# Kernel tuning notes

Hardware: AMD Instinct MI355X
Metric: run time of the kernel (lower is better)

Reference implementation:

```python
import jax, jax.numpy as jnp
import numpy as np

B, T, D, H, DK, DV = 2, 2048, 1024, 16, 64, 64
MODEL_SIZE = 1024
NEG_INF = -2.3819763e38
EPS = 1e-6
MAX_WAVELENGTH = 10000


def rms_norm(x, scale):
    # flax nn.RMSNorm over last axis, eps=1e-6, learned scale init to ones
    var = jnp.mean(jnp.square(x), axis=-1, keepdims=True)
    return x * jax.lax.rsqrt(var + EPS) * scale


def apply_rope(x):
    # x: [B, T, H, head_dim]
    *_, seq_len, num_heads, head_dim = x.shape
    fraction = 2 * jnp.arange(0, head_dim // 2) / head_dim
    timescale = MAX_WAVELENGTH ** fraction
    positions = jnp.arange(seq_len, dtype=x.dtype)
    sinusoid_inp = positions[:, None] / timescale[None, :]  # [T, head_dim//2]
    sinusoid_inp = sinusoid_inp[:, None, :]                 # [T, 1, head_dim//2]
    sin = jnp.sin(sinusoid_inp)
    cos = jnp.cos(sinusoid_inp)
    first_half, second_half = jnp.split(x, 2, axis=-1)
    first_part = first_half * cos - second_half * sin
    second_part = second_half * cos + first_half * sin
    return jnp.concatenate([first_part, second_part], axis=-1).astype(x.dtype)


def setup_inputs() -> dict:
    key = jax.random.key(0)
    ks = jax.random.split(key, 12)
    s = 0.02
    return {
        "query": jax.random.normal(ks[0], (B, T, D), jnp.float32),
        "key": jax.random.normal(ks[1], (B, T, D), jnp.float32),
        "value": jax.random.normal(ks[2], (B, T, D), jnp.float32),
        "mask": jnp.ones((B, H, T, T), dtype=bool),
        "Wq": jax.random.normal(ks[3], (D, H * DK), jnp.float32) * s,
        "bq": jnp.zeros((H * DK,), jnp.float32),
        "Wk": jax.random.normal(ks[4], (D, H * DK), jnp.float32) * s,
        "bk": jnp.zeros((H * DK,), jnp.float32),
        "Wv": jax.random.normal(ks[5], (D, H * DV), jnp.float32) * s,
        "bv": jnp.zeros((H * DV,), jnp.float32),
        "Wo": jax.random.normal(ks[6], (H * DV, MODEL_SIZE), jnp.float32) * s,
        "bo": jnp.zeros((MODEL_SIZE,), jnp.float32),
        "gq": jnp.ones((DK,), jnp.float32),
        "gk": jnp.ones((DK,), jnp.float32),
    }


def reference(query, key, value, mask, Wq, bq, Wk, bk, Wv, bv, Wo, bo, gq, gk):
    # Q/K projections with per-head RMSNorm then RoPE
    qh = (query @ Wq + bq).reshape(B, T, H, DK)
    qh = apply_rope(rms_norm(qh, gq))
    kh = (key @ Wk + bk).reshape(B, T, H, DK)
    kh = apply_rope(rms_norm(kh, gk))
    vh = (value @ Wv + bv).reshape(B, T, H, DV)

    logits = jnp.einsum("bthd,bThd->bhtT", qh, kh) / np.sqrt(DK).astype(query.dtype)
    logits = jnp.where(mask, logits, NEG_INF)
    weights = jax.nn.softmax(logits, axis=-1)
    weights = jnp.where(mask, weights, 0)
    attn = jnp.einsum("bhtT,bThd->bthd", weights, vh).reshape(B, T, H * DV)
    return attn @ Wo + bo
```

## Files before the change

kernel.cpp:

```cpp
#include <hip/hip_runtime.h>
#include <hip/hip_bf16.h>
#include <cstdint>
#include <cstddef>


typedef unsigned short ushort_t;
typedef unsigned int uint32;
typedef __bf16 bf16x8 __attribute__((ext_vector_type(8)));
typedef float f32x4 __attribute__((ext_vector_type(4)));

#define DEV static __device__ __forceinline__

DEV ushort_t f2bf(float f){
  uint32 x = __builtin_bit_cast(uint32, f);
  uint32 r = (x + 0x7fffu + ((x >> 16) & 1u)) >> 16;
  return (ushort_t)r;
}
DEV bf16x8 cvt8(f32x4 lo, f32x4 hi){
  bf16x8 r;
#pragma unroll
  for(int j=0;j<4;j++){ r[j] = (__bf16)lo[j]; r[j+4] = (__bf16)hi[j]; }
  return r;
}
DEV void gl_lds16(const ushort_t* g, ushort_t* l){
  __builtin_amdgcn_global_load_lds(
      (const __attribute__((address_space(1))) uint32*)g,
      (__attribute__((address_space(3))) uint32*)l, 16, 0, 0);
}

__global__ __launch_bounds__(256) void cvtbf(const float* __restrict__ x0,
                                             const float* __restrict__ x1,
                                             const float* __restrict__ x2,
                                             ushort_t* __restrict__ y0,
                                             ushort_t* __restrict__ y1,
                                             ushort_t* __restrict__ y2){
  int z = blockIdx.y;
  const float* x = (z==0)?x0:(z==1)?x1:x2;
  ushort_t* y    = (z==0)?y0:(z==1)?y1:y2;
  size_t i = ((size_t)blockIdx.x*256 + threadIdx.x)*8;
  f32x4 lo = *(const f32x4*)(x+i);
  f32x4 hi = *(const f32x4*)(x+i+4);
  *(bf16x8*)(y+i) = cvt8(lo, hi);
}

__global__ __launch_bounds__(256) void wtrans(const float* __restrict__ w0,
                                              const float* __restrict__ w1,
                                              const float* __restrict__ w2,
                                              const float* __restrict__ w3,
                                              ushort_t* __restrict__ wt){
  __shared__ float tile[64][65];
  int z = blockIdx.z;
  const float* W = (z==0)?w0:(z==1)?w1:(z==2)?w2:w3;
  ushort_t* O = wt + (size_t)z * (1024u*1024u);
  int kb = blockIdx.y * 64, nb = blockIdx.x * 64;
  int tr = threadIdx.x >> 4, tc = threadIdx.x & 15;
#pragma unroll
  for(int p=0;p<4;p++){
    int r = tr + p*16;
    f32x4 u = *(const f32x4*)(W + (size_t)(kb + r)*1024 + nb + tc*4);
    tile[r][tc*4+0]=u[0]; tile[r][tc*4+1]=u[1]; tile[r][tc*4+2]=u[2]; tile[r][tc*4+3]=u[3];
  }
  __syncthreads();
#pragma unroll
  for(int p=0;p<4;p++){
    int r = tr + p*16;
    ushort4 u;
    u.x = f2bf(tile[tc*4+0][r]); u.y = f2bf(tile[tc*4+1][r]);
    u.z = f2bf(tile[tc*4+2][r]); u.w = f2bf(tile[tc*4+3][r]);
    *(ushort4*)(O + (size_t)(nb + r)*1024 + kb + tc*4) = u;
  }
}

__global__ __launch_bounds__(256) void gemm128(
    const ushort_t* __restrict__ A0, const ushort_t* __restrict__ A1, const ushort_t* __restrict__ A2,
    const ushort_t* __restrict__ WT,
    const float* __restrict__ b0, const float* __restrict__ b1, const float* __restrict__ b2,
    ushort_t* __restrict__ O0, ushort_t* __restrict__ O1, ushort_t* __restrict__ O2,
    float* __restrict__ OF, int vtz, int f32z)
{
  __shared__ ushort_t As[128*32];
  __shared__ ushort_t Bs[128*32];
  const int K = 1024, N = 1024;
  int z = blockIdx.z;
  const ushort_t* A   = (z==0) ? A0 : (z==1) ? A1 : A2;
  const ushort_t* Bt  = WT + (size_t)z * (1024u*1024u);
  const float* bias   = (z==0) ? b0 : (z==1) ? b1 : b2;
  ushort_t* Cp        = (z==0) ? O0 : (z==1) ? O1 : O2;
  int rowBase = blockIdx.y * 128, colBase = blockIdx.x * 128;
  int tid = threadIdx.x, wave = tid >> 6, lane = tid & 63;
  int lr = lane & 15, lq = lane >> 4;
  int m0 = (wave & 1) * 64, n0 = (wave >> 1) * 64;
  int srow = wave*16 + (lane >> 2);
  int skc  = (lane & 3) * 8;
  const ushort_t* gA = A  + (size_t)(rowBase + srow)*K + skc;
  const ushort_t* gB = Bt + (size_t)(colBase + srow)*K + skc;
  ushort_t* lA = &As[srow*32 + skc];
  ushort_t* lB = &Bs[srow*32 + skc];
  f32x4 acc[4][4] = {};
  for(int kb = 0; kb < K; kb += 32){
    gl_lds16(gA + kb,          lA);
    gl_lds16(gA + kb + 64*K,   lA + 64*32);
    gl_lds16(gB + kb,          lB);
    gl_lds16(gB + kb + 64*K,   lB + 64*32);
    __syncthreads();
    bf16x8 af[4], bfr[4];
#pragma unroll
    for(int mi=0;mi<4;mi++) af[mi]  = *(const bf16x8*)&As[(m0 + mi*16 + lr)*32 + lq*8];
#pragma unroll
    for(int ni=0;ni<4;ni++) bfr[ni] = *(const bf16x8*)&Bs[(n0 + ni*16 + lr)*32 + lq*8];
#pragma unroll
    for(int mi=0;mi<4;mi++)
#pragma unroll
      for(int ni=0;ni<4;ni++)
        acc[mi][ni] = __builtin_amdgcn_mfma_f32_16x16x32_bf16(af[mi], bfr[ni], acc[mi][ni], 0,0,0);
    __syncthreads();
  }
  bool vt = (z == vtz);
  bool f32o = (z == f32z);
#pragma unroll
  for(int ni=0;ni<4;ni++){
    int col = colBase + n0 + ni*16 + lr;
    float bv = bias[col];
#pragma unroll
    for(int mi=0;mi<4;mi++){
      int row = rowBase + m0 + mi*16 + lq*4;
#pragma unroll
      for(int r=0;r<4;r++){
        float v = acc[mi][ni][r] + bv;
        if(f32o){
          OF[(size_t)(row + r)*N + col] = v;
        } else if(!vt){
          Cp[(size_t)(row + r)*N + col] = f2bf(v);
        } else {
          int rw = row + r;
          int bb = rw >> 11, t = rw & 2047, hh = col >> 6, dv = col & 63;
          Cp[((size_t)((bb*16 + hh)*64 + dv))*2048 + t] = f2bf(v);
        }
      }
    }
  }
}

__global__ __launch_bounds__(256) void rmsrope(ushort_t* __restrict__ QH, ushort_t* __restrict__ KH,
                                               const float* __restrict__ gq, const float* __restrict__ gk){
  int wave = threadIdx.x >> 6, lane = threadIdx.x & 63;
  int idx = blockIdx.x * 4 + wave;
  int s = idx >> 16;
  int rem = idx & 65535;
  ushort_t* P = s ? KH : QH;
  const float* G = s ? gk : gq;
  size_t base = (size_t)rem * 64;
  union { uint32 i; float f; } cv0; cv0.i = ((uint32)P[base + lane]) << 16;
  float x = cv0.f;
  float ss = x * x;
#pragma unroll
  for(int d=1; d<64; d<<=1) ss += __shfl_xor(ss, d, 64);
  float rn = rsqrtf(ss * (1.0f/64.0f) + 1e-6f);
  float xn = x * rn * G[lane];
  int i = lane & 31;
  int tpos = (rem >> 4) & 2047;
  float invts = exp2f((float)i * (-13.287712379549449f/32.0f));
  float ang = (float)tpos * invts;
  float sv, cvv;
  sincosf(ang, &sv, &cvv);
  float pr = __shfl_xor(xn, 32, 64);
  float out = (lane < 32) ? (xn*cvv - pr*sv) : (xn*cvv + pr*sv);
  P[base + lane] = f2bf(out);
}

__global__ __launch_bounds__(256, 2) void attn_k(const ushort_t* __restrict__ QH,
                                                 const ushort_t* __restrict__ KH,
                                                 const ushort_t* __restrict__ VT,
                                                 ushort_t* __restrict__ AT){
  __shared__ float sO[4][64][33];
  __shared__ float sM[4][32];
  __shared__ float sL[4][32];
  const float C = 0.18033688011112042f;
  int blk = blockIdx.x;
  int r5 = blk & 31;
  int bh = (r5 & 7)*4 + (r5 >> 3);
  int qt = blk >> 5;
  int b = bh >> 4, h = bh & 15;
  int q0 = qt * 64;
  int tid = threadIdx.x, wave = tid >> 6, lane = tid & 63;
  int lr = lane & 15, lq = lane >> 4;
  size_t tok0 = (size_t)b * 2048;

  bf16x8 qf[2][4];
#pragma unroll
  for(int ks=0;ks<2;ks++)
#pragma unroll
    for(int nt=0;nt<4;nt++){
      size_t e = ((tok0 + q0 + nt*16 + lr)*16 + h)*64 + (size_t)ks*32 + lq*8;
      qf[ks][nt] = *(const bf16x8*)(QH + e);
    }
  f32x4 o[4][4] = {};
  float m[4] = {-1e30f, -1e30f, -1e30f, -1e30f};
  float l[4] = {0.f, 0.f, 0.f, 0.f};
  size_t vbase = ((size_t)(b*16 + h) * 64) * 2048;

  for(int it=0; it<16; ++it){
    int kb = wave*512 + it*32;
    bf16x8 kA[2][2];
#pragma unroll
    for(int mt=0;mt<2;mt++)
#pragma unroll
      for(int ks=0;ks<2;ks++){
        size_t e = ((tok0 + kb + mt*16 + lr)*16 + h)*64 + (size_t)ks*32 + lq*8;
        kA[mt][ks] = *(const bf16x8*)(KH + e);
      }
    bf16x8 vA[4];
#pragma unroll
    for(int dvt=0;dvt<4;dvt++){
      size_t e = vbase + (size_t)(dvt*16 + lr)*2048 + kb + lq*8;
      vA[dvt] = *(const bf16x8*)(VT + e);
    }
    f32x4 s[2][4] = {};
#pragma unroll
    for(int ks=0;ks<2;ks++)
#pragma unroll
      for(int mt=0;mt<2;mt++)
#pragma unroll
        for(int nt=0;nt<4;nt++)
          s[mt][nt] = __builtin_amdgcn_mfma_f32_16x16x32_bf16(kA[mt][ks], qf[ks][nt], s[mt][nt], 0,0,0);

#pragma unroll
    for(int nt=0;nt<4;nt++){
      float mx = s[0][nt][0];
#pragma unroll
      for(int r=1;r<4;r++) mx = fmaxf(mx, s[0][nt][r]);
#pragma unroll
      for(int r=0;r<4;r++) mx = fmaxf(mx, s[1][nt][r]);
      mx = fmaxf(mx, __shfl_xor(mx, 16, 64));
      mx = fmaxf(mx, __shfl_xor(mx, 32, 64));
      float mn = fmaxf(m[nt], mx);
      float al = exp2f((m[nt] - mn) * C);
      m[nt] = mn;
      float rs = 0.f;
#pragma unroll
      for(int mt=0;mt<2;mt++)
#pragma unroll
        for(int r=0;r<4;r++){
          float p = exp2f((s[mt][nt][r] - mn) * C);
          s[mt][nt][r] = p;
          rs += p;
        }
      rs += __shfl_xor(rs, 16, 64);
      rs += __shfl_xor(rs, 32, 64);
      l[nt] = l[nt]*al + rs;
#pragma unroll
      for(int dvt=0;dvt<4;dvt++) o[dvt][nt] *= al;
    }
#pragma unroll
    for(int nt=0;nt<4;nt++){
      bf16x8 pB;
      int srcbase = lr + (lq & 1)*32;
#pragma unroll
      for(int j=0;j<8;j++){
        int src = srcbase + (j>>2)*16;
        float va = __shfl(s[0][nt][j&3], src, 64);
        float vb = __shfl(s[1][nt][j&3], src, 64);
        float pv = (lq >= 2) ? vb : va;
        pB[j] = (__bf16)pv;
      }
#pragma unroll
      for(int dvt=0;dvt<4;dvt++)
        o[dvt][nt] = __builtin_amdgcn_mfma_f32_16x16x32_bf16(vA[dvt], pB, o[dvt][nt], 0,0,0);
    }
  }
#pragma unroll
  for(int p=0;p<2;p++){
    __syncthreads();
#pragma unroll
    for(int ntl=0;ntl<2;ntl++){
      int nt = p*2 + ntl;
      if(lane < 16){ sM[wave][ntl*16+lane] = m[nt]; sL[wave][ntl*16+lane] = l[nt]; }
#pragma unroll
      for(int dvt=0;dvt<4;dvt++)
#pragma unroll
        for(int r=0;r<4;r++)
          sO[wave][dvt*16 + lq*4 + r][ntl*16 + lr] = o[dvt][nt][r];
    }
    __syncthreads();
    for(int e = tid; e < 2048; e += 256){
      int dv = e >> 5, qc = e & 31;
      float m0v = sM[0][qc], m1v = sM[1][qc], m2v = sM[2][qc], m3v = sM[3][qc];
      float msv = fmaxf(fmaxf(m0v,m1v), fmaxf(m2v,m3v));
      float w0 = exp2f((m0v-msv)*C), w1 = exp2f((m1v-msv)*C);
      float w2 = exp2f((m2v-msv)*C), w3 = exp2f((m3v-msv)*C);
      float L = sL[0][qc]*w0 + sL[1][qc]*w1 + sL[2][qc]*w2 + sL[3][qc]*w3;
      float O = sO[0][dv][qc]*w0 + sO[1][dv][qc]*w1 + sO[2][dv][qc]*w2 + sO[3][dv][qc]*w3;
      AT[(tok0 + q0 + p*32 + qc)*1024 + h*64 + dv] = f2bf(O / L);
    }
  }
}

extern "C" void kernel_launch(void* const* d_in, const int* in_sizes, int n_in,
                              void* d_out, int out_size, void* d_ws, size_t ws_size,
                              hipStream_t stream){
  (void)in_sizes; (void)n_in; (void)out_size; (void)ws_size;
  const float* q  = (const float*)d_in[0];
  const float* k  = (const float*)d_in[1];
  const float* v  = (const float*)d_in[2];
  const float* Wq = (const float*)d_in[4];
  const float* bq = (const float*)d_in[5];
  const float* Wk = (const float*)d_in[6];
  const float* bk = (const float*)d_in[7];
  const float* Wv = (const float*)d_in[8];
  const float* bv = (const float*)d_in[9];
  const float* Wo = (const float*)d_in[10];
  const float* bo = (const float*)d_in[11];
  const float* gq = (const float*)d_in[12];
  const float* gk = (const float*)d_in[13];
  char* ws = (char*)d_ws;
  ushort_t* WT = (ushort_t*)(ws);
  ushort_t* QB = (ushort_t*)(ws + (size_t)(16u<<20));
  ushort_t* KB = (ushort_t*)(ws + (size_t)(24u<<20));
  ushort_t* VB = (ushort_t*)(ws + (size_t)(32u<<20));
  ushort_t* QH = (ushort_t*)(ws + (size_t)(40u<<20));
  ushort_t* KH = (ushort_t*)(ws + (size_t)(48u<<20));
  ushort_t* VT = (ushort_t*)(ws + (size_t)(56u<<20));
  ushort_t* AT = (ushort_t*)(ws + (size_t)(64u<<20));
  float*    OUT = (float*)d_out;

  hipLaunchKernelGGL(cvtbf,   dim3(2048,3), dim3(256), 0, stream, q, k, v, QB, KB, VB);
  hipLaunchKernelGGL(wtrans,  dim3(16,16,4), dim3(256), 0, stream, Wq, Wk, Wv, Wo, WT);
  hipLaunchKernelGGL(gemm128, dim3(8,32,3),  dim3(256), 0, stream,
                     QB, KB, VB, WT, bq, bk, bv, QH, KH, VT, (float*)nullptr, 2, -1);
  hipLaunchKernelGGL(rmsrope, dim3(32768),   dim3(256), 0, stream, QH, KH, gq, gk);
  hipLaunchKernelGGL(attn_k,  dim3(1024),    dim3(256), 0, stream, QH, KH, VT, AT);
  hipLaunchKernelGGL(gemm128, dim3(8,32,1),  dim3(256), 0, stream,
                     AT, AT, AT, WT + (size_t)3*1024*1024, bo, bo, bo,
                     (ushort_t*)nullptr, (ushort_t*)nullptr, (ushort_t*)nullptr, OUT, -1, 0);
}
```

Before: 822.3 us.

## Fuse RMSNorm+RoPE into projection GEMM epilogue and tune attention inner loop

Removes the separate rmsrope kernel by applying per-head RMSNorm and RoPE directly in the Q/K projection GEMM epilogue, saving a read/write pass over QH and KH. In attention, the next K tile is prefetched during softmax, the running max is only rescaled when it grows past a threshold (lazy rescale), and P is packed to bf16 with v_cvt_pk and redistributed with ds_bpermute instead of per-element shuffles. The final reduction indexing is changed to make AT stores more contiguous. The lazy rescale relies on bounded exponent growth, and the register prefetch raises register pressure.

```diff
diff --git a/kernel.cpp b/kernel.cpp
--- a/kernel.cpp
+++ b/kernel.cpp
@@ -26,6 +26,11 @@
   __builtin_amdgcn_global_load_lds(
       (const __attribute__((address_space(1))) uint32*)g,
       (__attribute__((address_space(3))) uint32*)l, 16, 0, 0);
+}
+DEV uint32 cvtpk(float a, float b){
+  uint32 r;
+  asm("v_cvt_pk_bf16_f32 %0, %1, %2" : "=v"(r) : "v"(a), "v"(b));
+  return r;
 }
 
 __global__ __launch_bounds__(256) void cvtbf(const float* __restrict__ x0,
@@ -76,7 +81,8 @@
     const ushort_t* __restrict__ WT,
     const float* __restrict__ b0, const float* __restrict__ b1, const float* __restrict__ b2,
     ushort_t* __restrict__ O0, ushort_t* __restrict__ O1, ushort_t* __restrict__ O2,
-    float* __restrict__ OF, int vtz, int f32z)
+    float* __restrict__ OF, int vtz, int f32z,
+    const float* __restrict__ gq, const float* __restrict__ gk, int ropez)
 {
   __shared__ ushort_t As[128*32];
   __shared__ ushort_t Bs[128*32];
@@ -115,6 +121,47 @@
         acc[mi][ni] = __builtin_amdgcn_mfma_f32_16x16x32_bf16(af[mi], bfr[ni], acc[mi][ni], 0,0,0);
     __syncthreads();
   }
+  if(z < ropez){
+    const float* G = (z==0) ? gq : gk;
+    float g0 = G[lr], g1 = G[16+lr], g2 = G[32+lr], g3 = G[48+lr];
+    int cb = colBase + n0;
+    float bv0 = bias[cb+lr], bv1 = bias[cb+16+lr], bv2 = bias[cb+32+lr], bv3 = bias[cb+48+lr];
+    const float NC = -13.287712379549449f/32.0f;
+    float invt0 = exp2f((float)lr * NC);
+    float invt1 = exp2f((float)(16+lr) * NC);
+#pragma unroll
+    for(int mi=0;mi<4;mi++){
+#pragma unroll
+      for(int rr=0;rr<4;rr++){
+        int row = rowBase + m0 + mi*16 + lq*4 + rr;
+        float x0 = acc[mi][0][rr] + bv0;
+        float x1 = acc[mi][1][rr] + bv1;
+        float x2 = acc[mi][2][rr] + bv2;
+        float x3 = acc[mi][3][rr] + bv3;
+        float ss = x0*x0 + x1*x1 + x2*x2 + x3*x3;
+        ss += __shfl_xor(ss, 1, 64);
+        ss += __shfl_xor(ss, 2, 64);
+        ss += __shfl_xor(ss, 4, 64);
+        ss += __shfl_xor(ss, 8, 64);
+        float rn = rsqrtf(ss * (1.0f/64.0f) + 1e-6f);
+        x0 *= rn*g0; x1 *= rn*g1; x2 *= rn*g2; x3 *= rn*g3;
+        int tpos = row & 2047;
+        float s0, c0, s1, c1;
+        sincosf((float)tpos * invt0, &s0, &c0);
+        sincosf((float)tpos * invt1, &s1, &c1);
+        float o0 = x0*c0 - x2*s0;
+        float o1 = x1*c1 - x3*s1;
+        float o2 = x2*c0 + x0*s0;
+        float o3 = x3*c1 + x1*s1;
+        size_t rb = (size_t)row*N + cb + lr;
+        Cp[rb]    = f2bf(o0);
+        Cp[rb+16] = f2bf(o1);
+        Cp[rb+32] = f2bf(o2);
+        Cp[rb+48] = f2bf(o3);
+      }
+    }
+    return;
+  }
   bool vt = (z == vtz);
   bool f32o = (z == f32z);
 #pragma unroll
@@ -141,32 +188,13 @@
   }
 }
 
-__global__ __launch_bounds__(256) void rmsrope(ushort_t* __restrict__ QH, ushort_t* __restrict__ KH,
-                                               const float* __restrict__ gq, const float* __restrict__ gk){
-  int wave = threadIdx.x >> 6, lane = threadIdx.x & 63;
-  int idx = blockIdx.x * 4 + wave;
-  int s = idx >> 16;
-  int rem = idx & 65535;
-  ushort_t* P = s ? KH : QH;
-  const float* G = s ? gk : gq;
-  size_t base = (size_t)rem * 64;
-  union { uint32 i; float f; } cv0; cv0.i = ((uint32)P[base + lane]) << 16;
-  float x = cv0.f;
-  float ss = x * x;
-#pragma unroll
-  for(int d=1; d<64; d<<=1) ss += __shfl_xor(ss, d, 64);
-  float rn = rsqrtf(ss * (1.0f/64.0f) + 1e-6f);
-  float xn = x * rn * G[lane];
-  int i = lane & 31;
-  int tpos = (rem >> 4) & 2047;
-  float invts = exp2f((float)i * (-13.287712379549449f/32.0f));
-  float ang = (float)tpos * invts;
-  float sv, cvv;
-  sincosf(ang, &sv, &cvv);
-  float pr = __shfl_xor(xn, 32, 64);
-  float out = (lane < 32) ? (xn*cvv - pr*sv) : (xn*cvv + pr*sv);
-  P[base + lane] = f2bf(out);
-}
+#define LOADK(dst, KB_) do { \
+  _Pragma("unroll") \
+  for(int mt_=0;mt_<2;mt_++) \
+  _Pragma("unroll") \
+    for(int ks_=0;ks_<2;ks_++){ \
+      size_t e_ = ((tok0 + (KB_) + mt_*16 + lr)*16 + h)*64 + (size_t)ks_*32 + lq*8; \
+      dst[mt_][ks_] = *(const bf16x8*)(KH + e_); } } while(0)
 
 __global__ __launch_bounds__(256, 2) void attn_k(const ushort_t* __restrict__ QH,
                                                  const ushort_t* __restrict__ KH,
@@ -198,31 +226,30 @@
   float m[4] = {-1e30f, -1e30f, -1e30f, -1e30f};
   float l[4] = {0.f, 0.f, 0.f, 0.f};
   size_t vbase = ((size_t)(b*16 + h) * 64) * 2048;
+  int a0 = (lr + (lq & 1)*32) * 4;
+  int a1 = a0 + 64;
+  bool hi = (lq >= 2);
+
+  bf16x8 kA[2][2];
+  LOADK(kA, (size_t)(wave*512));
 
   for(int it=0; it<16; ++it){
     int kb = wave*512 + it*32;
-    bf16x8 kA[2][2];
-#pragma unroll
-    for(int mt=0;mt<2;mt++)
-#pragma unroll
-      for(int ks=0;ks<2;ks++){
-        size_t e = ((tok0 + kb + mt*16 + lr)*16 + h)*64 + (size_t)ks*32 + lq*8;
-        kA[mt][ks] = *(const bf16x8*)(KH + e);
-      }
+    f32x4 s[2][4] = {};
+#pragma unroll
+    for(int ks=0;ks<2;ks++)
+#pragma unroll
+      for(int mt=0;mt<2;mt++)
+#pragma unroll
+        for(int nt=0;nt<4;nt++)
+          s[mt][nt] = __builtin_amdgcn_mfma_f32_16x16x32_bf16(kA[mt][ks], qf[ks][nt], s[mt][nt], 0,0,0);
+
     bf16x8 vA[4];
 #pragma unroll
     for(int dvt=0;dvt<4;dvt++){
       size_t e = vbase + (size_t)(dvt*16 + lr)*2048 + kb + lq*8;
       vA[dvt] = *(const bf16x8*)(VT + e);
     }
-    f32x4 s[2][4] = {};
-#pragma unroll
-    for(int ks=0;ks<2;ks++)
-#pragma unroll
-      for(int mt=0;mt<2;mt++)
-#pragma unroll
-        for(int nt=0;nt<4;nt++)
-          s[mt][nt] = __builtin_amdgcn_mfma_f32_16x16x32_bf16(kA[mt][ks], qf[ks][nt], s[mt][nt], 0,0,0);
 
 #pragma unroll
     for(int nt=0;nt<4;nt++){
@@ -233,39 +260,53 @@
       for(int r=0;r<4;r++) mx = fmaxf(mx, s[1][nt][r]);
       mx = fmaxf(mx, __shfl_xor(mx, 16, 64));
       mx = fmaxf(mx, __shfl_xor(mx, 32, 64));
-      float mn = fmaxf(m[nt], mx);
-      float al = exp2f((m[nt] - mn) * C);
-      m[nt] = mn;
+      if(__any((mx - m[nt]) * C > 4.0f)){
+        float mn = fmaxf(m[nt], mx);
+        float al = exp2f((m[nt] - mn) * C);
+        m[nt] = mn;
+        l[nt] *= al;
+#pragma unroll
+        for(int dvt=0;dvt<4;dvt++) o[dvt][nt] *= al;
+      }
+      float mC = m[nt] * C;
       float rs = 0.f;
 #pragma unroll
       for(int mt=0;mt<2;mt++)
 #pragma unroll
         for(int r=0;r<4;r++){
-          float p = exp2f((s[mt][nt][r] - mn) * C);
+          float p = exp2f(s[mt][nt][r]*C - mC);
           s[mt][nt][r] = p;
           rs += p;
         }
       rs += __shfl_xor(rs, 16, 64);
       rs += __shfl_xor(rs, 32, 64);
-      l[nt] = l[nt]*al + rs;
-#pragma unroll
-      for(int dvt=0;dvt<4;dvt++) o[dvt][nt] *= al;
-    }
+      l[nt] += rs;
+    }
+
+    if(it < 15) LOADK(kA, (size_t)(kb + 32));
+
 #pragma unroll
     for(int nt=0;nt<4;nt++){
-      bf16x8 pB;
-      int srcbase = lr + (lq & 1)*32;
-#pragma unroll
-      for(int j=0;j<8;j++){
-        int src = srcbase + (j>>2)*16;
-        float va = __shfl(s[0][nt][j&3], src, 64);
-        float vb = __shfl(s[1][nt][j&3], src, 64);
-        float pv = (lq >= 2) ? vb : va;
-        pB[j] = (__bf16)pv;
-      }
+      uint32 pk0 = cvtpk(s[0][nt][0], s[0][nt][1]);
+      uint32 pk1 = cvtpk(s[0][nt][2], s[0][nt][3]);
+      uint32 pk2 = cvtpk(s[1][nt][0], s[1][nt][1]);
+      uint32 pk3 = cvtpk(s[1][nt][2], s[1][nt][3]);
+      uint32 w0a = (uint32)__builtin_amdgcn_ds_bpermute(a0, (int)pk0);
+      uint32 w0b = (uint32)__builtin_amdgcn_ds_bpermute(a0, (int)pk2);
+      uint32 w1a = (uint32)__builtin_amdgcn_ds_bpermute(a0, (int)pk1);
+      uint32 w1b = (uint32)__builtin_amdgcn_ds_bpermute(a0, (int)pk3);
+      uint32 w2a = (uint32)__builtin_amdgcn_ds_bpermute(a1, (int)pk0);
+      uint32 w2b = (uint32)__builtin_amdgcn_ds_bpermute(a1, (int)pk2);
+      uint32 w3a = (uint32)__builtin_amdgcn_ds_bpermute(a1, (int)pk1);
+      uint32 w3b = (uint32)__builtin_amdgcn_ds_bpermute(a1, (int)pk3);
+      union { uint32 u[4]; bf16x8 v; } pu;
+      pu.u[0] = hi ? w0b : w0a;
+      pu.u[1] = hi ? w1b : w1a;
+      pu.u[2] = hi ? w2b : w2a;
+      pu.u[3] = hi ? w3b : w3a;
 #pragma unroll
       for(int dvt=0;dvt<4;dvt++)
-        o[dvt][nt] = __builtin_amdgcn_mfma_f32_16x16x32_bf16(vA[dvt], pB, o[dvt][nt], 0,0,0);
+        o[dvt][nt] = __builtin_amdgcn_mfma_f32_16x16x32_bf16(vA[dvt], pu.v, o[dvt][nt], 0,0,0);
     }
   }
 #pragma unroll
@@ -283,7 +324,7 @@
     }
     __syncthreads();
     for(int e = tid; e < 2048; e += 256){
-      int dv = e >> 5, qc = e & 31;
+      int dv = e & 63, qc = e >> 6;
       float m0v = sM[0][qc], m1v = sM[1][qc], m2v = sM[2][qc], m3v = sM[3][qc];
       float msv = fmaxf(fmaxf(m0v,m1v), fmaxf(m2v,m3v));
       float w0 = exp2f((m0v-msv)*C), w1 = exp2f((m1v-msv)*C);
@@ -326,10 +367,11 @@
   hipLaunchKernelGGL(cvtbf,   dim3(2048,3), dim3(256), 0, stream, q, k, v, QB, KB, VB);
   hipLaunchKernelGGL(wtrans,  dim3(16,16,4), dim3(256), 0, stream, Wq, Wk, Wv, Wo, WT);
   hipLaunchKernelGGL(gemm128, dim3(8,32,3),  dim3(256), 0, stream,
-                     QB, KB, VB, WT, bq, bk, bv, QH, KH, VT, (float*)nullptr, 2, -1);
-  hipLaunchKernelGGL(rmsrope, dim3(32768),   dim3(256), 0, stream, QH, KH, gq, gk);
+                     QB, KB, VB, WT, bq, bk, bv, QH, KH, VT, (float*)nullptr, 2, -1,
+                     gq, gk, 2);
   hipLaunchKernelGGL(attn_k,  dim3(1024),    dim3(256), 0, stream, QH, KH, VT, AT);
   hipLaunchKernelGGL(gemm128, dim3(8,32,1),  dim3(256), 0, stream,
                      AT, AT, AT, WT + (size_t)3*1024*1024, bo, bo, bo,
-                     (ushort_t*)nullptr, (ushort_t*)nullptr, (ushort_t*)nullptr, OUT, -1, 0);
-}
+                     (ushort_t*)nullptr, (ushort_t*)nullptr, (ushort_t*)nullptr, OUT, -1, 0,
+                     gq, gk, 0);
+}
```

Measured after the change: 800.9 us. -2.6%, faster.
